# Optimization experiments

Measured on AMD Instinct MI355X. Metric: run time of the kernel, lower is better.

Reference implementation:

```python
import jax, jax.numpy as jnp
import numpy as np

B, S, H, L = 4, 2048, 1024, 4
CLAMP_LO, CLAMP_HI = 1e-8, 1.0 - 1e-8
LN_EPS = 1e-5


def setup_inputs() -> dict:
    key = jax.random.key(0)
    ks = jax.random.split(key, 13)
    s = 1.0 / np.sqrt(H)
    u = lambda k, shape: jax.random.uniform(k, shape, jnp.float32, -s, s)
    return {
        "x": jax.random.normal(ks[0], (B, S, H), jnp.float32),
        "fwd_Wz": u(ks[1], (L, H, H)), "fwd_bz": u(ks[2], (L, H)),
        "fwd_Wh": u(ks[3], (L, H, H)), "fwd_bh": u(ks[4], (L, H)),
        "bwd_Wz": u(ks[5], (L, H, H)), "bwd_bz": u(ks[6], (L, H)),
        "bwd_Wh": u(ks[7], (L, H, H)), "bwd_bh": u(ks[8], (L, H)),
        "fusion_W": u(ks[9], (H, 2 * H)), "fusion_b": u(ks[10], (H,)),
        "ln_gamma": jnp.ones((H,), jnp.float32),
        "ln_beta": jnp.zeros((H,), jnp.float32),
    }


def _linear_scan(a, b):
    # h_t = a_t * h_{t-1} + b_t over axis 1 (seq), via associative scan.
    # composition: (a2,b2) o (a1,b1) = (a2*a1, a2*b1 + b2)
    def combine(left, right):
        al, bl = left
        ar, br = right
        return (ar * al, ar * bl + br)
    _, h = jax.lax.associative_scan(combine, (a, b), axis=1)
    return h


def _mingru(x, Wz, bz, Wh, bh):
    # x: (B,S,H); Wz,Wh: (H_out,H_in) like nn.Linear
    z = jax.nn.sigmoid(jnp.einsum('bsi,hi->bsh', x, Wz) + bz)
    h_tilde = jnp.tanh(jnp.einsum('bsi,hi->bsh', x, Wh) + bh)
    a = jnp.clip(1.0 - z, CLAMP_LO, CLAMP_HI)
    return _linear_scan(a, z * h_tilde)


def _layernorm(x, gamma, beta):
    mu = jnp.mean(x, axis=-1, keepdims=True)
    var = jnp.mean(jnp.square(x - mu), axis=-1, keepdims=True)
    return (x - mu) * jax.lax.rsqrt(var + LN_EPS) * gamma + beta


def _stack(x, Wz, bz, Wh, bh, gamma, beta):
    h = x
    for i in range(L):
        h_new = _mingru(h, Wz[i], bz[i], Wh[i], bh[i])
        if i > 0:
            h_new = h_new + h  # residual (shapes match for i>0)
        h = _layernorm(h_new, gamma, beta)
    return h


def reference(x, fwd_Wz, fwd_bz, fwd_Wh, fwd_bh,
              bwd_Wz, bwd_bz, bwd_Wh, bwd_bh,
              fusion_W, fusion_b, ln_gamma, ln_beta):
    h_fwd = _stack(x, fwd_Wz, fwd_bz, fwd_Wh, fwd_bh, ln_gamma, ln_beta)
    h_bwd = _stack(jnp.flip(x, axis=1), bwd_Wz, bwd_bz, bwd_Wh, bwd_bh,
                   ln_gamma, ln_beta)
    h_bwd = jnp.flip(h_bwd, axis=1)
    h_comb = jnp.concatenate([h_fwd, h_bwd], axis=-1)  # (B,S,2H)
    return jnp.einsum('bsi,hi->bsh', h_comb, fusion_W) + fusion_b
```

## Files before the change

### kernel.cpp

```cpp
#include <hip/hip_runtime.h>
#include <stdint.h>

#define Bn 4
#define Sn 2048
#define Hn 1024
#define Ln 4
#define Mn (Bn*Sn)
#define CHUNK 32
#define NCH (Sn/CHUNK)

typedef __bf16 bf16x8 __attribute__((ext_vector_type(8)));
typedef float  f32x4  __attribute__((ext_vector_type(4)));
typedef uint32_t u32;

__device__ __forceinline__ unsigned short f2bf(float f) {
  uint32_t u = __float_as_uint(f);
  uint32_t r = (u + 0x7FFFu + ((u >> 16) & 1u)) >> 16;
  return (unsigned short)r;
}
__device__ __forceinline__ float bf2f(unsigned short u) {
  return __uint_as_float(((uint32_t)u) << 16);
}

__device__ __forceinline__ void gload_lds16(const void* g, void* l) {
  __builtin_amdgcn_global_load_lds((const __attribute__((address_space(1))) void*)g,
                                   (__attribute__((address_space(3))) void*)l, 16, 0, 0);
}

__global__ __launch_bounds__(256) void cast_f32_bf16(const float* __restrict__ src,
                                                     unsigned short* __restrict__ dst, int n4) {
  int i = blockIdx.x * 256 + threadIdx.x;
  if (i >= n4) return;
  float4 v = reinterpret_cast<const float4*>(src)[i];
  ushort4 o;
  o.x = f2bf(v.x); o.y = f2bf(v.y); o.z = f2bf(v.z); o.w = f2bf(v.w);
  reinterpret_cast<ushort4*>(dst)[i] = o;
}


#define DSR(d, b, imm) \
  asm volatile("ds_read_b128 %0, %1 offset:%c2" : "=&v"(d) : "v"(b), "i"(imm))

#define VMW(n) do { \
    asm volatile("s_waitcnt vmcnt(" #n ")"); \
    __builtin_amdgcn_sched_barrier(0); \
  } while (0)

#define LGKM(n) do { \
    asm volatile("s_waitcnt lgkmcnt(" #n ")"); \
    __builtin_amdgcn_sched_barrier(0); \
  } while (0)

#define DSR4(ARR, base, off) do { \
    DSR(ARR[0], base, (off)); \
    DSR(ARR[1], base, (off) + 1024); \
    DSR(ARR[2], base, (off) + 2048); \
    DSR(ARR[3], base, (off) + 3072); \
  } while (0)

#define CL(ARR, BARR, MB) do { \
    __builtin_amdgcn_s_setprio(1); \
    _Pragma("unroll") \
    for (int _m = 0; _m < 4; ++_m) { \
      _Pragma("unroll") \
      for (int _n = 0; _n < 4; ++_n) \
        acc[(MB) + _m][_n] = __builtin_amdgcn_mfma_f32_16x16x32_bf16( \
            ARR[_m], BARR[_n], acc[(MB) + _m][_n], 0, 0, 0); \
    } \
    __builtin_amdgcn_s_setprio(0); \
  } while (0)

#define BODY(buf) do { \
    if constexpr (MF == 8) { \
      DSR4(aA, baseA, ((buf) * 2 + 0) * RGA); \
      DSR4(b0, baseB, ((buf) * 2 + 0) * 16384); \
      DSR4(aB, baseA, ((buf) * 2 + 0) * RGA + 4096); \
      LGKM(4); \
      CL(aA, b0, 0); \
      DSR4(b1, baseB, ((buf) * 2 + 1) * 16384); \
      LGKM(4); \
      CL(aB, b0, 4); \
      DSR4(aA, baseA, ((buf) * 2 + 1) * RGA); \
      LGKM(4); \
      DSR4(aB, baseA, ((buf) * 2 + 1) * RGA + 4096); \
      LGKM(4); \
      CL(aA, b1, 0); \
      LGKM(0); \
      CL(aB, b1, 4); \
    } else { \
      DSR4(aA, baseA, ((buf) * 2 + 0) * RGA); \
      DSR4(b0, baseB, ((buf) * 2 + 0) * 16384); \
      DSR4(aB, baseA, ((buf) * 2 + 1) * RGA); \
      LGKM(4); \
      CL(aA, b0, 0); \
      DSR4(b1, baseB, ((buf) * 2 + 1) * 16384); \
      LGKM(0); \
      CL(aB, b1, 0); \
    } \
  } while (0)

template<int MF>
__global__ __launch_bounds__(512, 2) void gemm_t(
    const unsigned short* __restrict__ act,
    const unsigned short* __restrict__ Wlo,
    const unsigned short* __restrict__ Whi,
    const float* __restrict__ bias0, const float* __restrict__ bias1,
    int Nsplit, float* __restrict__ out, unsigned short* __restrict__ outbf,
    int Ndim, int K) {
  constexpr int BMR = MF * 32;
  constexpr int RGA = BMR * 64;
  __shared__ unsigned char smA[4 * RGA];
  __shared__ unsigned char smB[65536];
  const int tid  = threadIdx.x;
  const int lane = tid & 63;
  const int w    = tid >> 6;
  const int waveM = w >> 2;
  const int waveN = w & 3;
  const int bm = blockIdx.x, bn = blockIdx.y;

  const unsigned short* Wp; int nbase;
  if (bn * 256 < Nsplit) { Wp = Wlo; nbase = bn * 256; }
  else                   { Wp = Whi; nbase = bn * 256 - Nsplit; }

  const int swz  = (((lane >> 4) ^ ((lane >> 1) & 3)) << 4);
  const int aoff = (waveM * (MF * 16) + (lane & 15)) * 64 + swz;
  const int boff = (waveN * 64 + (lane & 15)) * 64 + swz;

  const u32 baseA = (u32)(size_t)(void*)&smA[0] + (u32)aoff;
  const u32 baseB = (u32)(size_t)(void*)&smB[0] + (u32)boff;

  const int srow = tid >> 2;
  const int slog = (tid & 3) ^ ((srow >> 1) & 3);
  const unsigned short* aS0 = act + (size_t)(bm * BMR + srow) * K + slog * 8;
  const unsigned short* aS1 = aS0 + (size_t)128 * K;
  const unsigned short* bS0 = Wp  + (size_t)(nbase + srow) * K + slog * 8;
  const unsigned short* bS1 = bS0 + (size_t)128 * K;
  const int wB = w * 1024;

  f32x4 acc[MF][4];
#pragma unroll
  for (int m = 0; m < MF; ++m)
#pragma unroll
    for (int n = 0; n < 4; ++n) acc[m][n] = (f32x4)0.0f;

  bf16x8 aA[4], aB[4], b0[4], b1[4];

  auto STG4 = [&](int t, int buf) {
#pragma unroll
    for (int kh = 0; kh < 2; ++kh) {
      unsigned char* ra = smA + (buf * 2 + kh) * RGA;
      gload_lds16(aS0 + (size_t)t * 64 + kh * 32, ra + wB);
      if constexpr (MF == 8)
        gload_lds16(aS1 + (size_t)t * 64 + kh * 32, ra + 8192 + wB);
      unsigned char* rb = smB + (buf * 2 + kh) * 16384;
      gload_lds16(bS0 + (size_t)t * 64 + kh * 32, rb + wB);
      gload_lds16(bS1 + (size_t)t * 64 + kh * 32, rb + 8192 + wB);
    }
  };

  const int nkt   = K >> 6;
  const int niter = nkt >> 1;

  STG4(0, 0);
  VMW(0);
  __builtin_amdgcn_s_barrier();

  for (int j = 0; j < niter - 1; ++j) {
    STG4(2 * j + 1, 1); BODY(0); VMW(0); __builtin_amdgcn_s_barrier();
    STG4(2 * j + 2, 0); BODY(1); VMW(0); __builtin_amdgcn_s_barrier();
  }
  STG4(nkt - 1, 1); BODY(0); VMW(0); __builtin_amdgcn_s_barrier();
  BODY(1);

  const int colBase = bn * 256 + waveN * 64;
  const int rowBase = bm * BMR + waveM * (MF * 16);
#pragma unroll
  for (int m = 0; m < MF; ++m) {
#pragma unroll
    for (int n = 0; n < 4; ++n) {
      int col = colBase + n * 16 + (lane & 15);
      float bv = (col < Nsplit) ? bias0[col] : bias1[col - Nsplit];
      if (outbf) {
#pragma unroll
        for (int r = 0; r < 4; ++r) {
          int row = rowBase + m * 16 + (lane >> 4) * 4 + r;
          outbf[(size_t)row * Ndim + col] = f2bf(acc[m][n][r] + bv);
        }
      } else {
#pragma unroll
        for (int r = 0; r < 4; ++r) {
          int row = rowBase + m * 16 + (lane >> 4) * 4 + r;
          out[(size_t)row * Ndim + col] = acc[m][n][r] + bv;
        }
      }
    }
  }
}

__device__ __forceinline__ void gate_ab(float zp, float hp, float& a, float& bv) {
  float z  = 1.0f / (1.0f + __expf(-zp));
  float e  = __expf(-2.0f * fabsf(hp));
  float th = (1.0f - e) / (1.0f + e);
  th = (hp >= 0.0f) ? th : -th;
  a  = fminf(fmaxf(1.0f - z, 1e-8f), 1.0f - 1e-8f);
  bv = z * th;
}

__global__ __launch_bounds__(256) void scan_p1(const unsigned short* __restrict__ pre,
                                               float* __restrict__ Ac, float* __restrict__ Bc,
                                               int dir) {
  int tid = threadIdx.x;
  int bid = blockIdx.x;
  int ht = bid & 3;
  int c  = (bid >> 2) & (NCH - 1);
  int b  = bid >> 8;
  int h  = ht * 256 + tid;
  float Aa = 1.0f, Bb = 0.0f;
  for (int j = 0; j < CHUNK; ++j) {
    int t = c * CHUNK + j;
    int s = dir ? (Sn - 1 - t) : t;
    const unsigned short* p = pre + (size_t)(b * Sn + s) * 2048;
    float a, bv;
    gate_ab(bf2f(p[h]), bf2f(p[1024 + h]), a, bv);
    Aa = a * Aa;
    Bb = a * Bb + bv;
  }
  Ac[(size_t)(b * NCH + c) * Hn + h] = Aa;
  Bc[(size_t)(b * NCH + c) * Hn + h] = Bb;
}

__global__ __launch_bounds__(256) void scan_mid(const float* __restrict__ Ac,
                                                const float* __restrict__ Bc,
                                                float* __restrict__ pref) {
  int tid = blockIdx.x * 256 + threadIdx.x;
  int b = tid >> 10;
  int h = tid & 1023;
  float run = 0.0f;
  for (int c = 0; c < NCH; ++c) {
    size_t idx = (size_t)(b * NCH + c) * Hn + h;
    pref[idx] = run;
    run = Ac[idx] * run + Bc[idx];
  }
}

__global__ __launch_bounds__(1024) void scan_p3_ln(
    const unsigned short* __restrict__ pre, const float* __restrict__ pref,
    const unsigned short* __restrict__ resid,
    const float* __restrict__ gamma, const float* __restrict__ beta,
    unsigned short* __restrict__ out_bf,
    int bf_stride, int bf_off, int dir) {
  __shared__ unsigned short hsl[CHUNK][Hn];
  const int h = threadIdx.x;
  const int c = blockIdx.x & (NCH - 1);
  const int b = blockIdx.x >> 6;
  float hprev = pref[(size_t)(b * NCH + c) * Hn + h];

  for (int j = 0; j < CHUNK; ++j) {
    int t = c * CHUNK + j;
    int s = dir ? (Sn - 1 - t) : t;
    const unsigned short* p = pre + (size_t)(b * Sn + s) * 2048;
    float a, bv;
    gate_ab(bf2f(p[h]), bf2f(p[1024 + h]), a, bv);
    hprev = a * hprev + bv;
    hsl[j][h] = f2bf(hprev);
  }
  __syncthreads();

  const int lane = h & 63;
  const int wv   = h >> 6;
  float gm[16], bt[16];
  {
    const float4* gp = reinterpret_cast<const float4*>(gamma);
    const float4* bp = reinterpret_cast<const float4*>(beta);
#pragma unroll
    for (int half = 0; half < 2; ++half) {
      int base = half * 128 + lane * 2;
#pragma unroll
      for (int i = 0; i < 2; ++i) {
        float4 g4 = gp[base + i], b4 = bp[base + i];
        int o = half * 8 + i * 4;
        gm[o+0] = g4.x; gm[o+1] = g4.y; gm[o+2] = g4.z; gm[o+3] = g4.w;
        bt[o+0] = b4.x; bt[o+1] = b4.y; bt[o+2] = b4.z; bt[o+3] = b4.w;
      }
    }
  }

  for (int rr = 0; rr < 2; ++rr) {
    const int j = wv * 2 + rr;
    const int t = c * CHUNK + j;
    const int s = dir ? (Sn - 1 - t) : t;
    const size_t row = (size_t)(b * Sn + s);

    const uint4* rp = reinterpret_cast<const uint4*>(&hsl[j][0]);
    uint4 q0 = rp[lane], q1 = rp[64 + lane];
    uint32_t uw[8] = {q0.x, q0.y, q0.z, q0.w, q1.x, q1.y, q1.z, q1.w};
    float v[16];
#pragma unroll
    for (int k = 0; k < 8; ++k) {
      v[2*k]   = bf2f((unsigned short)(uw[k] & 0xffffu));
      v[2*k+1] = bf2f((unsigned short)(uw[k] >> 16));
    }
    if (resid) {
      const uint4* rf = reinterpret_cast<const uint4*>(resid + row * Hn);
      uint4 r0 = rf[lane], r1 = rf[64 + lane];
      uint32_t rw[8] = {r0.x, r0.y, r0.z, r0.w, r1.x, r1.y, r1.z, r1.w};
#pragma unroll
      for (int k = 0; k < 8; ++k) {
        v[2*k]   += bf2f((unsigned short)(rw[k] & 0xffffu));
        v[2*k+1] += bf2f((unsigned short)(rw[k] >> 16));
      }
    }
    float s1 = 0.0f, s2 = 0.0f;
#pragma unroll
    for (int m = 0; m < 16; ++m) { s1 += v[m]; s2 += v[m] * v[m]; }
#pragma unroll
    for (int off = 1; off < 64; off <<= 1) {
      s1 += __shfl_xor(s1, off);
      s2 += __shfl_xor(s2, off);
    }
    float mu  = s1 * (1.0f / Hn);
    float var = s2 * (1.0f / Hn) - mu * mu;
    float rs  = rsqrtf(var + 1e-5f);

    float o[16];
#pragma unroll
    for (int m = 0; m < 16; ++m) o[m] = (v[m] - mu) * rs * gm[m] + bt[m];

    uint4* ob = reinterpret_cast<uint4*>(out_bf + row * bf_stride + bf_off);
    uint4 w0, w1;
    w0.x = f2bf(o[0])  | ((u32)f2bf(o[1])  << 16);
    w0.y = f2bf(o[2])  | ((u32)f2bf(o[3])  << 16);
    w0.z = f2bf(o[4])  | ((u32)f2bf(o[5])  << 16);
    w0.w = f2bf(o[6])  | ((u32)f2bf(o[7])  << 16);
    w1.x = f2bf(o[8])  | ((u32)f2bf(o[9])  << 16);
    w1.y = f2bf(o[10]) | ((u32)f2bf(o[11]) << 16);
    w1.z = f2bf(o[12]) | ((u32)f2bf(o[13]) << 16);
    w1.w = f2bf(o[14]) | ((u32)f2bf(o[15]) << 16);
    ob[lane]      = w0;
    ob[64 + lane] = w1;
  }
}

extern "C" void kernel_launch(void* const* d_in, const int* in_sizes, int n_in,
                              void* d_out, int out_size, void* d_ws, size_t ws_size,
                              hipStream_t stream) {
  const float* x        = (const float*)d_in[0];
  const float* fwd_Wz   = (const float*)d_in[1];
  const float* fwd_bz   = (const float*)d_in[2];
  const float* fwd_Wh   = (const float*)d_in[3];
  const float* fwd_bh   = (const float*)d_in[4];
  const float* bwd_Wz   = (const float*)d_in[5];
  const float* bwd_bz   = (const float*)d_in[6];
  const float* bwd_Wh   = (const float*)d_in[7];
  const float* bwd_bh   = (const float*)d_in[8];
  const float* fusion_W = (const float*)d_in[9];
  const float* fusion_b = (const float*)d_in[10];
  const float* gamma    = (const float*)d_in[11];
  const float* beta     = (const float*)d_in[12];
  float* out = (float*)d_out;

  unsigned short* WzA    = (unsigned short*)d_ws;
  unsigned short* WhA    = WzA + 8ULL * 1024 * 1024;
  unsigned short* fusWbf = WhA + 8ULL * 1024 * 1024;
  unsigned short* xbf    = fusWbf + 2ULL * 1024 * 1024;
  unsigned short* actbf  = xbf + 8ULL * 1024 * 1024;
  unsigned short* combbf = actbf + 8ULL * 1024 * 1024;
  float* actf = (float*)(combbf + 16ULL * 1024 * 1024);
  float* pre  = actf + 8ULL * 1024 * 1024;
  float* hs   = pre + 16ULL * 1024 * 1024;
  float* Ac   = hs + 8ULL * 1024 * 1024;
  float* Bc   = Ac + (size_t)Bn * NCH * Hn;
  float* pref = Bc + (size_t)Bn * NCH * Hn;
  size_t need = (size_t)((char*)(pref + (size_t)Bn * NCH * Hn) - (char*)d_ws);
  if (ws_size < need) return;
  unsigned short* prebf = (unsigned short*)pre;

  auto cast = [&](const float* src, unsigned short* dst, size_t n) {
    int n4 = (int)(n / 4);
    cast_f32_bf16<<<(n4 + 255) / 256, 256, 0, stream>>>(src, dst, n4);
  };
  cast(fwd_Wz, WzA,                     4ULL * 1024 * 1024);
  cast(bwd_Wz, WzA + 4ULL * 1024 * 1024, 4ULL * 1024 * 1024);
  cast(fwd_Wh, WhA,                     4ULL * 1024 * 1024);
  cast(bwd_Wh, WhA + 4ULL * 1024 * 1024, 4ULL * 1024 * 1024);
  cast(fusion_W, fusWbf, 2ULL * 1024 * 1024);
  cast(x, xbf, 8ULL * 1024 * 1024);

  for (int d = 0; d < 2; ++d) {
    const float* bz = d ? bwd_bz : fwd_bz;
    const float* bh = d ? bwd_bh : fwd_bh;
    for (int l = 0; l < Ln; ++l) {
      const unsigned short* a_in = (l == 0) ? xbf : actbf;
      const unsigned short* Wlo = WzA + (size_t)(d * 4 + l) * 1024 * 1024;
      const unsigned short* Whi = WhA + (size_t)(d * 4 + l) * 1024 * 1024;
      gemm_t<8><<<dim3(Mn / 256, 2048 / 256), 512, 0, stream>>>(
          a_in, Wlo, Whi, bz + l * 1024, bh + l * 1024, 1024,
          nullptr, prebf, 2048, 1024);
      scan_p1<<<Bn * NCH * 4, 256, 0, stream>>>(prebf, Ac, Bc, d);
      scan_mid<<<16, 256, 0, stream>>>(Ac, Bc, pref);
      if (l < Ln - 1)
        scan_p3_ln<<<Bn * NCH, 1024, 0, stream>>>(
            prebf, pref, (l == 0) ? nullptr : actbf, gamma, beta,
            actbf, 1024, 0, d);
      else
        scan_p3_ln<<<Bn * NCH, 1024, 0, stream>>>(
            prebf, pref, actbf, gamma, beta,
            combbf, 2048, d * 1024, d);
    }
  }
  gemm_t<4><<<dim3(Mn / 128, 1024 / 256), 512, 0, stream>>>(
      combbf, fusWbf, fusWbf, fusion_b, fusion_b, 1 << 30, out, nullptr, 1024, 2048);
}
```

Measured before the change: 710.5 us.

## Fuse chunk-prefix scan into scan_p3, merge weight casts, vectorize scan lanes

Removes the separate scan_mid kernel: each scan_p3_ln block now recomputes its own chunk prefix by serially combining the preceding chunks' (A,B) aggregates, loaded eight at a time. scan_p1 and scan_p3_ln now handle two hidden channels per thread with 32-bit bf16 pair loads, and scan_p3_ln drops to 512 threads per block. The six cast launches are merged into one cast_all kernel. This cuts launch count and the serial single-pass mid kernel, at the cost of redundant prefix work that grows with chunk index and fewer threads per block.

```diff
diff --git a/kernel.cpp b/kernel.cpp
--- a/kernel.cpp
+++ b/kernel.cpp
@@ -27,14 +27,25 @@
                                    (__attribute__((address_space(3))) void*)l, 16, 0, 0);
 }
 
-__global__ __launch_bounds__(256) void cast_f32_bf16(const float* __restrict__ src,
-                                                     unsigned short* __restrict__ dst, int n4) {
-  int i = blockIdx.x * 256 + threadIdx.x;
-  if (i >= n4) return;
-  float4 v = reinterpret_cast<const float4*>(src)[i];
+__global__ __launch_bounds__(256) void cast_all(
+    const float* __restrict__ s0, const float* __restrict__ s1,
+    const float* __restrict__ s2, const float* __restrict__ s3,
+    const float* __restrict__ s4, const float* __restrict__ s5,
+    unsigned short* __restrict__ d0, unsigned short* __restrict__ d1,
+    unsigned short* __restrict__ d2, unsigned short* __restrict__ d3,
+    unsigned short* __restrict__ d4, unsigned short* __restrict__ d5) {
+  long i = (long)blockIdx.x * 256 + threadIdx.x;
+  const float* s; unsigned short* d; long off;
+  if      (i < 1048576) { s = s0; d = d0; off = i; }
+  else if (i < 2097152) { s = s1; d = d1; off = i - 1048576; }
+  else if (i < 3145728) { s = s2; d = d2; off = i - 2097152; }
+  else if (i < 4194304) { s = s3; d = d3; off = i - 3145728; }
+  else if (i < 4718592) { s = s4; d = d4; off = i - 4194304; }
+  else                  { s = s5; d = d5; off = i - 4718592; }
+  float4 v = reinterpret_cast<const float4*>(s)[off];
   ushort4 o;
   o.x = f2bf(v.x); o.y = f2bf(v.y); o.z = f2bf(v.z); o.w = f2bf(v.w);
-  reinterpret_cast<ushort4*>(dst)[i] = o;
+  reinterpret_cast<ushort4*>(d)[off] = o;
 }
 
 
@@ -211,63 +222,84 @@
                                                int dir) {
   int tid = threadIdx.x;
   int bid = blockIdx.x;
-  int ht = bid & 3;
-  int c  = (bid >> 2) & (NCH - 1);
-  int b  = bid >> 8;
-  int h  = ht * 256 + tid;
-  float Aa = 1.0f, Bb = 0.0f;
+  int ht = bid & 1;
+  int c  = (bid >> 1) & (NCH - 1);
+  int b  = bid >> 7;
+  int h0 = ht * 512 + tid * 2;
+  float A0 = 1.0f, B0 = 0.0f, A1 = 1.0f, B1 = 0.0f;
   for (int j = 0; j < CHUNK; ++j) {
     int t = c * CHUNK + j;
     int s = dir ? (Sn - 1 - t) : t;
     const unsigned short* p = pre + (size_t)(b * Sn + s) * 2048;
+    u32 zp = *reinterpret_cast<const u32*>(p + h0);
+    u32 hp = *reinterpret_cast<const u32*>(p + 1024 + h0);
     float a, bv;
-    gate_ab(bf2f(p[h]), bf2f(p[1024 + h]), a, bv);
-    Aa = a * Aa;
-    Bb = a * Bb + bv;
-  }
-  Ac[(size_t)(b * NCH + c) * Hn + h] = Aa;
-  Bc[(size_t)(b * NCH + c) * Hn + h] = Bb;
-}
-
-__global__ __launch_bounds__(256) void scan_mid(const float* __restrict__ Ac,
-                                                const float* __restrict__ Bc,
-                                                float* __restrict__ pref) {
-  int tid = blockIdx.x * 256 + threadIdx.x;
-  int b = tid >> 10;
-  int h = tid & 1023;
-  float run = 0.0f;
-  for (int c = 0; c < NCH; ++c) {
-    size_t idx = (size_t)(b * NCH + c) * Hn + h;
-    pref[idx] = run;
-    run = Ac[idx] * run + Bc[idx];
-  }
-}
-
-__global__ __launch_bounds__(1024) void scan_p3_ln(
-    const unsigned short* __restrict__ pre, const float* __restrict__ pref,
+    gate_ab(bf2f((unsigned short)(zp & 0xffffu)), bf2f((unsigned short)(hp & 0xffffu)), a, bv);
+    A0 = a * A0; B0 = a * B0 + bv;
+    gate_ab(bf2f((unsigned short)(zp >> 16)), bf2f((unsigned short)(hp >> 16)), a, bv);
+    A1 = a * A1; B1 = a * B1 + bv;
+  }
+  size_t idx = (size_t)(b * NCH + c) * Hn + h0;
+  *reinterpret_cast<float2*>(&Ac[idx]) = make_float2(A0, A1);
+  *reinterpret_cast<float2*>(&Bc[idx]) = make_float2(B0, B1);
+}
+
+__global__ __launch_bounds__(512) void scan_p3_ln(
+    const unsigned short* __restrict__ pre,
+    const float* __restrict__ Ac, const float* __restrict__ Bc,
     const unsigned short* __restrict__ resid,
     const float* __restrict__ gamma, const float* __restrict__ beta,
     unsigned short* __restrict__ out_bf,
     int bf_stride, int bf_off, int dir) {
   __shared__ unsigned short hsl[CHUNK][Hn];
-  const int h = threadIdx.x;
-  const int c = blockIdx.x & (NCH - 1);
-  const int b = blockIdx.x >> 6;
-  float hprev = pref[(size_t)(b * NCH + c) * Hn + h];
+  const int tid = threadIdx.x;
+  const int h0  = tid * 2;
+  const int c   = blockIdx.x & (NCH - 1);
+  const int b   = blockIdx.x >> 6;
+
+  float r0 = 0.0f, r1 = 0.0f;
+  {
+    int cc = 0;
+    for (; cc + 8 <= c; cc += 8) {
+      float2 A2[8], B2[8];
+#pragma unroll
+      for (int q = 0; q < 8; ++q) {
+        size_t idx = (size_t)(b * NCH + cc + q) * Hn + h0;
+        A2[q] = *reinterpret_cast<const float2*>(&Ac[idx]);
+        B2[q] = *reinterpret_cast<const float2*>(&Bc[idx]);
+      }
+#pragma unroll
+      for (int q = 0; q < 8; ++q) {
+        r0 = A2[q].x * r0 + B2[q].x;
+        r1 = A2[q].y * r1 + B2[q].y;
+      }
+    }
+    for (; cc < c; ++cc) {
+      size_t idx = (size_t)(b * NCH + cc) * Hn + h0;
+      float2 A2 = *reinterpret_cast<const float2*>(&Ac[idx]);
+      float2 B2 = *reinterpret_cast<const float2*>(&Bc[idx]);
+      r0 = A2.x * r0 + B2.x;
+      r1 = A2.y * r1 + B2.y;
+    }
+  }
 
   for (int j = 0; j < CHUNK; ++j) {
     int t = c * CHUNK + j;
     int s = dir ? (Sn - 1 - t) : t;
     const unsigned short* p = pre + (size_t)(b * Sn + s) * 2048;
+    u32 zp = *reinterpret_cast<const u32*>(p + h0);
+    u32 hp = *reinterpret_cast<const u32*>(p + 1024 + h0);
     float a, bv;
-    gate_ab(bf2f(p[h]), bf2f(p[1024 + h]), a, bv);
-    hprev = a * hprev + bv;
-    hsl[j][h] = f2bf(hprev);
+    gate_ab(bf2f((unsigned short)(zp & 0xffffu)), bf2f((unsigned short)(hp & 0xffffu)), a, bv);
+    r0 = a * r0 + bv;
+    gate_ab(bf2f((unsigned short)(zp >> 16)), bf2f((unsigned short)(hp >> 16)), a, bv);
+    r1 = a * r1 + bv;
+    *reinterpret_cast<u32*>(&hsl[j][h0]) = (u32)f2bf(r0) | ((u32)f2bf(r1) << 16);
   }
   __syncthreads();
 
-  const int lane = h & 63;
-  const int wv   = h >> 6;
+  const int lane = tid & 63;
+  const int wv   = tid >> 6;
   float gm[16], bt[16];
   {
     const float4* gp = reinterpret_cast<const float4*>(gamma);
@@ -285,8 +317,8 @@
     }
   }
 
-  for (int rr = 0; rr < 2; ++rr) {
-    const int j = wv * 2 + rr;
+  for (int rr = 0; rr < 4; ++rr) {
+    const int j = wv * 4 + rr;
     const int t = c * CHUNK + j;
     const int s = dir ? (Sn - 1 - t) : t;
     const size_t row = (size_t)(b * Sn + s);
@@ -302,8 +334,8 @@
     }
     if (resid) {
       const uint4* rf = reinterpret_cast<const uint4*>(resid + row * Hn);
-      uint4 r0 = rf[lane], r1 = rf[64 + lane];
-      uint32_t rw[8] = {r0.x, r0.y, r0.z, r0.w, r1.x, r1.y, r1.z, r1.w};
+      uint4 r0v = rf[lane], r1v = rf[64 + lane];
+      uint32_t rw[8] = {r0v.x, r0v.y, r0v.z, r0v.w, r1v.x, r1v.y, r1v.z, r1v.w};
 #pragma unroll
       for (int k = 0; k < 8; ++k) {
         v[2*k]   += bf2f((unsigned short)(rw[k] & 0xffffu));
@@ -375,16 +407,9 @@
   if (ws_size < need) return;
   unsigned short* prebf = (unsigned short*)pre;
 
-  auto cast = [&](const float* src, unsigned short* dst, size_t n) {
-    int n4 = (int)(n / 4);
-    cast_f32_bf16<<<(n4 + 255) / 256, 256, 0, stream>>>(src, dst, n4);
-  };
-  cast(fwd_Wz, WzA,                     4ULL * 1024 * 1024);
-  cast(bwd_Wz, WzA + 4ULL * 1024 * 1024, 4ULL * 1024 * 1024);
-  cast(fwd_Wh, WhA,                     4ULL * 1024 * 1024);
-  cast(bwd_Wh, WhA + 4ULL * 1024 * 1024, 4ULL * 1024 * 1024);
-  cast(fusion_W, fusWbf, 2ULL * 1024 * 1024);
-  cast(x, xbf, 8ULL * 1024 * 1024);
+  cast_all<<<26624, 256, 0, stream>>>(
+      fwd_Wz, bwd_Wz, fwd_Wh, bwd_Wh, fusion_W, x,
+      WzA, WzA + 4ULL * 1024 * 1024, WhA, WhA + 4ULL * 1024 * 1024, fusWbf, xbf);
 
   for (int d = 0; d < 2; ++d) {
     const float* bz = d ? bwd_bz : fwd_bz;
@@ -396,15 +421,14 @@
       gemm_t<8><<<dim3(Mn / 256, 2048 / 256), 512, 0, stream>>>(
           a_in, Wlo, Whi, bz + l * 1024, bh + l * 1024, 1024,
           nullptr, prebf, 2048, 1024);
-      scan_p1<<<Bn * NCH * 4, 256, 0, stream>>>(prebf, Ac, Bc, d);
-      scan_mid<<<16, 256, 0, stream>>>(Ac, Bc, pref);
+      scan_p1<<<Bn * NCH * 2, 256, 0, stream>>>(prebf, Ac, Bc, d);
       if (l < Ln - 1)
-        scan_p3_ln<<<Bn * NCH, 1024, 0, stream>>>(
-            prebf, pref, (l == 0) ? nullptr : actbf, gamma, beta,
+        scan_p3_ln<<<Bn * NCH, 512, 0, stream>>>(
+            prebf, Ac, Bc, (l == 0) ? nullptr : actbf, gamma, beta,
             actbf, 1024, 0, d);
       else
-        scan_p3_ln<<<Bn * NCH, 1024, 0, stream>>>(
-            prebf, pref, actbf, gamma, beta,
+        scan_p3_ln<<<Bn * NCH, 512, 0, stream>>>(
+            prebf, Ac, Bc, actbf, gamma, beta,
             combbf, 2048, d * 1024, d);
     }
   }
```

After: 756.0 us. 1.06x slower.

## Fuse cast kernels into one launch and fold chunk-prefix scan into scan_p3

Applied to the files above, without the earlier changes.

Merges the six separate f32-to-bf16 cast launches into a single kernel that picks its source and destination by global index range. It also removes the scan_mid kernel: each scan_p3_ln block now recomputes its own carry-in prefix by serially combining all previous chunk (A,B) pairs, with loads batched in groups of 8. This drops 8 tiny serial scan_mid launches (16 blocks each) and the pref buffer round trip. In exchange it adds redundant prefix work, up to 63 chunk steps per block, which later chunks pay as extra latency.

```diff
diff --git a/kernel.cpp b/kernel.cpp
--- a/kernel.cpp
+++ b/kernel.cpp
@@ -27,14 +27,25 @@
                                    (__attribute__((address_space(3))) void*)l, 16, 0, 0);
 }
 
-__global__ __launch_bounds__(256) void cast_f32_bf16(const float* __restrict__ src,
-                                                     unsigned short* __restrict__ dst, int n4) {
-  int i = blockIdx.x * 256 + threadIdx.x;
-  if (i >= n4) return;
-  float4 v = reinterpret_cast<const float4*>(src)[i];
+__global__ __launch_bounds__(256) void cast_all(
+    const float* __restrict__ s0, const float* __restrict__ s1,
+    const float* __restrict__ s2, const float* __restrict__ s3,
+    const float* __restrict__ s4, const float* __restrict__ s5,
+    unsigned short* __restrict__ d0, unsigned short* __restrict__ d1,
+    unsigned short* __restrict__ d2, unsigned short* __restrict__ d3,
+    unsigned short* __restrict__ d4, unsigned short* __restrict__ d5) {
+  long i = (long)blockIdx.x * 256 + threadIdx.x;
+  const float* s; unsigned short* d; long off;
+  if      (i < 1048576) { s = s0; d = d0; off = i; }
+  else if (i < 2097152) { s = s1; d = d1; off = i - 1048576; }
+  else if (i < 3145728) { s = s2; d = d2; off = i - 2097152; }
+  else if (i < 4194304) { s = s3; d = d3; off = i - 3145728; }
+  else if (i < 4718592) { s = s4; d = d4; off = i - 4194304; }
+  else                  { s = s5; d = d5; off = i - 4718592; }
+  float4 v = reinterpret_cast<const float4*>(s)[off];
   ushort4 o;
   o.x = f2bf(v.x); o.y = f2bf(v.y); o.z = f2bf(v.z); o.w = f2bf(v.w);
-  reinterpret_cast<ushort4*>(dst)[i] = o;
+  reinterpret_cast<ushort4*>(d)[off] = o;
 }
 
 
@@ -229,22 +240,9 @@
   Bc[(size_t)(b * NCH + c) * Hn + h] = Bb;
 }
 
-__global__ __launch_bounds__(256) void scan_mid(const float* __restrict__ Ac,
-                                                const float* __restrict__ Bc,
-                                                float* __restrict__ pref) {
-  int tid = blockIdx.x * 256 + threadIdx.x;
-  int b = tid >> 10;
-  int h = tid & 1023;
-  float run = 0.0f;
-  for (int c = 0; c < NCH; ++c) {
-    size_t idx = (size_t)(b * NCH + c) * Hn + h;
-    pref[idx] = run;
-    run = Ac[idx] * run + Bc[idx];
-  }
-}
-
 __global__ __launch_bounds__(1024) void scan_p3_ln(
-    const unsigned short* __restrict__ pre, const float* __restrict__ pref,
+    const unsigned short* __restrict__ pre,
+    const float* __restrict__ Ac, const float* __restrict__ Bc,
     const unsigned short* __restrict__ resid,
     const float* __restrict__ gamma, const float* __restrict__ beta,
     unsigned short* __restrict__ out_bf,
@@ -253,7 +251,26 @@
   const int h = threadIdx.x;
   const int c = blockIdx.x & (NCH - 1);
   const int b = blockIdx.x >> 6;
-  float hprev = pref[(size_t)(b * NCH + c) * Hn + h];
+
+  float hprev = 0.0f;
+  {
+    int cc = 0;
+    for (; cc + 8 <= c; cc += 8) {
+      float Af[8], Bf[8];
+#pragma unroll
+      for (int q = 0; q < 8; ++q) {
+        size_t idx = (size_t)(b * NCH + cc + q) * Hn + h;
+        Af[q] = Ac[idx];
+        Bf[q] = Bc[idx];
+      }
+#pragma unroll
+      for (int q = 0; q < 8; ++q) hprev = Af[q] * hprev + Bf[q];
+    }
+    for (; cc < c; ++cc) {
+      size_t idx = (size_t)(b * NCH + cc) * Hn + h;
+      hprev = Ac[idx] * hprev + Bc[idx];
+    }
+  }
 
   for (int j = 0; j < CHUNK; ++j) {
     int t = c * CHUNK + j;
@@ -302,8 +319,8 @@
     }
     if (resid) {
       const uint4* rf = reinterpret_cast<const uint4*>(resid + row * Hn);
-      uint4 r0 = rf[lane], r1 = rf[64 + lane];
-      uint32_t rw[8] = {r0.x, r0.y, r0.z, r0.w, r1.x, r1.y, r1.z, r1.w};
+      uint4 r0v = rf[lane], r1v = rf[64 + lane];
+      uint32_t rw[8] = {r0v.x, r0v.y, r0v.z, r0v.w, r1v.x, r1v.y, r1v.z, r1v.w};
 #pragma unroll
       for (int k = 0; k < 8; ++k) {
         v[2*k]   += bf2f((unsigned short)(rw[k] & 0xffffu));
@@ -375,16 +392,9 @@
   if (ws_size < need) return;
   unsigned short* prebf = (unsigned short*)pre;
 
-  auto cast = [&](const float* src, unsigned short* dst, size_t n) {
-    int n4 = (int)(n / 4);
-    cast_f32_bf16<<<(n4 + 255) / 256, 256, 0, stream>>>(src, dst, n4);
-  };
-  cast(fwd_Wz, WzA,                     4ULL * 1024 * 1024);
-  cast(bwd_Wz, WzA + 4ULL * 1024 * 1024, 4ULL * 1024 * 1024);
-  cast(fwd_Wh, WhA,                     4ULL * 1024 * 1024);
-  cast(bwd_Wh, WhA + 4ULL * 1024 * 1024, 4ULL * 1024 * 1024);
-  cast(fusion_W, fusWbf, 2ULL * 1024 * 1024);
-  cast(x, xbf, 8ULL * 1024 * 1024);
+  cast_all<<<26624, 256, 0, stream>>>(
+      fwd_Wz, bwd_Wz, fwd_Wh, bwd_Wh, fusion_W, x,
+      WzA, WzA + 4ULL * 1024 * 1024, WhA, WhA + 4ULL * 1024 * 1024, fusWbf, xbf);
 
   for (int d = 0; d < 2; ++d) {
     const float* bz = d ? bwd_bz : fwd_bz;
@@ -397,14 +407,13 @@
           a_in, Wlo, Whi, bz + l * 1024, bh + l * 1024, 1024,
           nullptr, prebf, 2048, 1024);
       scan_p1<<<Bn * NCH * 4, 256, 0, stream>>>(prebf, Ac, Bc, d);
-      scan_mid<<<16, 256, 0, stream>>>(Ac, Bc, pref);
       if (l < Ln - 1)
         scan_p3_ln<<<Bn * NCH, 1024, 0, stream>>>(
-            prebf, pref, (l == 0) ? nullptr : actbf, gamma, beta,
+            prebf, Ac, Bc, (l == 0) ? nullptr : actbf, gamma, beta,
             actbf, 1024, 0, d);
       else
         scan_p3_ln<<<Bn * NCH, 1024, 0, stream>>>(
-            prebf, pref, actbf, gamma, beta,
+            prebf, Ac, Bc, actbf, gamma, beta,
             combbf, 2048, d * 1024, d);
     }
   }
```

Result: faster. 681.0 us (-4.2%).
